# Performance work log

Measured on AMD Instinct MI355X. Metric: run time of the kernel, lower is better.

Reference implementation:

```python
import jax, jax.numpy as jnp
import numpy as np


def _blended_linear(h, W, b, blend):
    # Equivalent to building w[b] = sum_e blend[e,b]*W[e] (shape B,out,in)
    # and computing w[b] @ h[b] + sum_e blend[e,b]*b[e], without the huge
    # per-sample weight tensor.
    # h: (B, in), W: (E, out, in), b: (E, out), blend: (E, B) -> (B, out)
    y = jnp.einsum('eoi,bi->ebo', W, h)          # per-expert outputs
    y = jnp.einsum('eb,ebo->bo', blend, y)       # blend across experts
    return y + blend.T @ b                       # blended bias


def setup_inputs() -> dict:
    key = jax.random.key(0)
    ks = jax.random.split(key, 9)
    E, B = 8, 8192
    dims = [480, 512, 512, 363]
    inp = {
        'x': jax.random.normal(ks[0], (B, dims[0]), jnp.float32),
        'weight_blend': jax.random.uniform(ks[1], (E, B), jnp.float32),
        'W1': jax.random.normal(ks[2], (E, dims[1], dims[0]), jnp.float32) * 0.05,
        'b1': jax.random.normal(ks[3], (E, dims[1]), jnp.float32) * 0.05,
        'W2': jax.random.normal(ks[4], (E, dims[2], dims[1]), jnp.float32) * 0.05,
        'b2': jax.random.normal(ks[5], (E, dims[2]), jnp.float32) * 0.05,
        'W3': jax.random.normal(ks[6], (E, dims[3], dims[2]), jnp.float32) * 0.05,
        'b3': jax.random.normal(ks[7], (E, dims[3]), jnp.float32) * 0.05,
        'batch_size': B,
    }
    return inp


def reference(x, weight_blend, W1, b1, W2, b2, W3, b3, batch_size):
    # Dropout layers are identity in eval mode; final_ac=True -> softmax.
    h = _blended_linear(x, W1, b1, weight_blend)
    h = jax.nn.elu(h)
    h = _blended_linear(h, W2, b2, weight_blend)
    h = jax.nn.elu(h)
    h = _blended_linear(h, W3, b3, weight_blend)
    return jax.nn.softmax(h, axis=-1)
```

## Files before the change

kernel.cpp:

```cpp
#include <hip/hip_runtime.h>
#include <cstdint>

#define E_EXP 8
#define BATCH 8192
#define D0 480
#define D1 512
#define D2 512
#define D3 363
#define KP 512
#define N3PAD 384

typedef _Float16 f16x8 __attribute__((ext_vector_type(8)));
typedef float f32x4 __attribute__((ext_vector_type(4)));
typedef unsigned short u16;
typedef u16 u16x8 __attribute__((ext_vector_type(8)));

__device__ __forceinline__ u16 f2h(float f) {
    _Float16 h = (_Float16)f;
    return __builtin_bit_cast(u16, h);
}

__device__ __forceinline__ void async16(const u16* g, u16* s) {
    __builtin_amdgcn_global_load_lds(
        reinterpret_cast<const __attribute__((address_space(1))) void*>(
            reinterpret_cast<uintptr_t>(g)),
        reinterpret_cast<__attribute__((address_space(3))) void*>(
            reinterpret_cast<uintptr_t>(s)),
        16, 0, 0);
}

__device__ __forceinline__ void pack_seg(const float* __restrict__ src,
                                         u16* __restrict__ dst,
                                         int OUT_src, int OUTP, int IN_src) {
    int total = E_EXP * OUTP * 128;
    int in4 = IN_src >> 2;
    for (int idx = blockIdx.x * blockDim.x + threadIdx.x; idx < total;
         idx += gridDim.x * blockDim.x) {
        int e = idx / (OUTP * 128);
        int r = idx - e * OUTP * 128;
        int o = r >> 7;
        int k4 = r & 127;
        ushort4 w;
        if (o < OUT_src && k4 < in4) {
            const float4 v = *reinterpret_cast<const float4*>(
                src + ((size_t)e * OUT_src + o) * IN_src + (k4 << 2));
            w.x = f2h(v.x); w.y = f2h(v.y); w.z = f2h(v.z); w.w = f2h(v.w);
        } else {
            w.x = 0; w.y = 0; w.z = 0; w.w = 0;
        }
        *reinterpret_cast<ushort4*>(dst + ((size_t)e * OUTP + o) * KP + (k4 << 2)) = w;
    }
}

__global__ void pack_all(const float* __restrict__ W1, const float* __restrict__ W2,
                         const float* __restrict__ W3, u16* __restrict__ wf1,
                         u16* __restrict__ wf2, u16* __restrict__ wf3) {
    pack_seg(W1, wf1, 512, 512, D0);
    pack_seg(W2, wf2, 512, 512, D1);
    pack_seg(W3, wf3, D3, N3PAD, D2);
}

__global__ void pad_x(const float* __restrict__ x, u16* __restrict__ xp) {
    int total = BATCH * 128;
    for (int idx = blockIdx.x * blockDim.x + threadIdx.x; idx < total;
         idx += gridDim.x * blockDim.x) {
        int b = idx >> 7, k4 = idx & 127;
        ushort4 w;
        if (k4 < 120) {
            const float4 v = *reinterpret_cast<const float4*>(
                x + (size_t)b * D0 + (k4 << 2));
            w.x = f2h(v.x); w.y = f2h(v.y); w.z = f2h(v.z); w.w = f2h(v.w);
        } else {
            w.x = 0; w.y = 0; w.z = 0; w.w = 0;
        }
        *reinterpret_cast<ushort4*>(xp + (size_t)b * KP + (k4 << 2)) = w;
    }
}

__global__ __launch_bounds__(512, 2) void gemm_all(
    const u16* __restrict__ A, const u16* __restrict__ Bw,
    const float* __restrict__ blend, const float* __restrict__ bias,
    u16* __restrict__ out, int OUTP, int OUTR, int nbn, int mode) {
    __shared__ __align__(16) u16 S[49152];
    const int tid = threadIdx.x;
    const int w = tid >> 6, lane = tid & 63;
    const int wm2 = w & 3, wn2 = w >> 2;
    const int q = lane >> 4, l15 = lane & 15;

    const int id = blockIdx.x;
    const int xcd = id & 7;
    const int j = id >> 3;
    const int bm = ((j & 3) << 3) + xcd;
    const int bn = j >> 2;

    f32x4 acc[4][2];
#pragma unroll
    for (int mi = 0; mi < 4; ++mi)
#pragma unroll
        for (int ni = 0; ni < 2; ++ni) acc[mi][ni] = (f32x4){0.f, 0.f, 0.f, 0.f};

    _Float16 blh[8][4];
#pragma unroll
    for (int e = 0; e < 8; ++e)
#pragma unroll
        for (int mi = 0; mi < 4; ++mi)
            blh[e][mi] = (_Float16)blend[e * BATCH + bm * 256 + wm2 * 64 +
                                         mi * 16 + l15];

    const int l4r = lane >> 2;
    const int l4s = lane & 3;
    const int ks8 = (l4s ^ (l4r & 3)) << 3;
    const size_t EST = (size_t)OUTP * KP;
    const u16* gA0 = A + (size_t)(bm * 256 + w * 32 + l4r) * KP + ks8;
    const u16* gB0 = Bw + (size_t)w * EST + (size_t)(bn * 64 + l4r) * KP + ks8;
    const size_t R16 = (size_t)16 * KP;
    const int aBase = w * 1024;
    const int bBase = 8192 + w * 2048;

    const int ra = (q ^ (l15 & 3)) << 3;
    const int arow[4] = {(wm2 * 64 + 0 * 16 + l15) * 32 + ra,
                         (wm2 * 64 + 1 * 16 + l15) * 32 + ra,
                         (wm2 * 64 + 2 * 16 + l15) * 32 + ra,
                         (wm2 * 64 + 3 * 16 + l15) * 32 + ra};
    const int brow0 = (wn2 * 32 + l15) * 32 + ra;
    const int brow1 = (wn2 * 32 + 16 + l15) * 32 + ra;

    auto stage = [&](int kt, int p) {
        const int ko = kt << 5;
        u16* buf = S + p * 24576;
        async16(gA0 + ko, buf + aBase);
        async16(gA0 + R16 + ko, buf + aBase + 512);
        async16(gB0 + ko, buf + bBase);
        async16(gB0 + R16 + ko, buf + bBase + 512);
        async16(gB0 + 2 * R16 + ko, buf + bBase + 1024);
        async16(gB0 + 3 * R16 + ko, buf + bBase + 1536);
    };

    stage(0, 0);
    __syncthreads();

#pragma unroll 2
    for (int kt = 0; kt < 16; ++kt) {
        const int p = kt & 1;
        if (kt < 15) stage(kt + 1, p ^ 1);
        const u16* As_ = S + p * 24576;
        const u16* Bs_ = As_ + 8192;
        f16x8 af[4];
#pragma unroll
        for (int mi = 0; mi < 4; ++mi)
            af[mi] = *reinterpret_cast<const f16x8*>(&As_[arow[mi]]);
#pragma unroll
        for (int e = 0; e < 8; ++e) {
            f16x8 bf0 = *reinterpret_cast<const f16x8*>(&Bs_[e * 2048 + brow0]);
            f16x8 bf1 = *reinterpret_cast<const f16x8*>(&Bs_[e * 2048 + brow1]);
#pragma unroll
            for (int mi = 0; mi < 4; ++mi) {
                f16x8 as = af[mi] * blh[e][mi];
                acc[mi][0] = __builtin_amdgcn_mfma_f32_16x16x32_f16(
                    as, bf0, acc[mi][0], 0, 0, 0);
                acc[mi][1] = __builtin_amdgcn_mfma_f32_16x16x32_f16(
                    as, bf1, acc[mi][1], 0, 0, 0);
            }
        }
        __syncthreads();
    }

    float* Blf = reinterpret_cast<float*>(S);
    float* Bif = reinterpret_cast<float*>(S + 16384);
    for (int idx = tid; idx < 2048; idx += 512) {
        int e = idx >> 8, r = idx & 255;
        Blf[r * 8 + e] = blend[e * BATCH + bm * 256 + r];
    }
    {
        int e = tid >> 6, c = tid & 63;
        int cg = bn * 64 + c;
        Bif[c * 8 + e] = (cg < OUTR) ? bias[e * OUTR + cg] : 0.f;
    }
    __syncthreads();
#pragma unroll
    for (int mi = 0; mi < 4; ++mi) {
#pragma unroll
        for (int ni = 0; ni < 2; ++ni) {
            int col_l = wn2 * 32 + ni * 16 + l15;
            int gcol = bn * 64 + col_l;
#pragma unroll
            for (int r = 0; r < 4; ++r) {
                int rl = wm2 * 64 + mi * 16 + q * 4 + r;
                float bb = 0.f;
#pragma unroll
                for (int e = 0; e < 8; ++e)
                    bb += Blf[rl * 8 + e] * Bif[col_l * 8 + e];
                float v = acc[mi][ni][r] + bb;
                if (mode == 0) v = v > 0.f ? v : expm1f(v);
                out[(size_t)(bm * 256 + rl) * OUTP + gcol] = f2h(v);
            }
        }
    }
}

__global__ __launch_bounds__(128) void softmax_rows(
    const u16* __restrict__ P, float* __restrict__ out) {
    const int b = blockIdx.x;
    const int tid = threadIdx.x, lane = tid & 63, w = tid >> 6;
    float v[3];
    int n = 0;
    float mx = -3.4e38f;
    for (int i = tid; i < D3; i += 128) {
        float s = (float)*reinterpret_cast<const _Float16*>(
            P + (size_t)b * N3PAD + i);
        v[n] = s; mx = fmaxf(mx, s); ++n;
    }
#pragma unroll
    for (int off = 32; off >= 1; off >>= 1) mx = fmaxf(mx, __shfl_xor(mx, off, 64));
    __shared__ float sm[4];
    if (lane == 0) sm[w] = mx;
    __syncthreads();
    mx = fmaxf(sm[0], sm[1]);
    float s = 0.f;
    for (int jj = 0; jj < n; ++jj) { v[jj] = expf(v[jj] - mx); s += v[jj]; }
#pragma unroll
    for (int off = 32; off >= 1; off >>= 1) s += __shfl_xor(s, off, 64);
    if (lane == 0) sm[2 + w] = s;
    __syncthreads();
    float inv = 1.f / (sm[2] + sm[3]);
    n = 0;
    for (int i = tid; i < D3; i += 128) { out[(size_t)b * D3 + i] = v[n] * inv; ++n; }
}

extern "C" void kernel_launch(void* const* d_in, const int* in_sizes, int n_in,
                              void* d_out, int out_size, void* d_ws, size_t ws_size,
                              hipStream_t stream) {
    const float* x = (const float*)d_in[0];
    const float* blend = (const float*)d_in[1];
    const float* W1 = (const float*)d_in[2];
    const float* b1 = (const float*)d_in[3];
    const float* W2 = (const float*)d_in[4];
    const float* b2 = (const float*)d_in[5];
    const float* W3 = (const float*)d_in[6];
    const float* b3 = (const float*)d_in[7];
    float* outp = (float*)d_out;

    char* ws = (char*)d_ws;
    u16* wf1 = (u16*)ws; ws += (size_t)E_EXP * 512 * KP * 2;
    u16* wf2 = (u16*)ws; ws += (size_t)E_EXP * 512 * KP * 2;
    u16* wf3 = (u16*)ws; ws += (size_t)E_EXP * N3PAD * KP * 2;
    u16* xp = (u16*)ws;  ws += (size_t)BATCH * KP * 2;
    u16* h1 = (u16*)ws;  ws += (size_t)BATCH * KP * 2;
    u16* h2 = (u16*)ws;  ws += (size_t)BATCH * KP * 2;
    u16* P = (u16*)ws;

    pack_all<<<1024, 256, 0, stream>>>(W1, W2, W3, wf1, wf2, wf3);
    pad_x<<<2048, 256, 0, stream>>>(x, xp);

    gemm_all<<<32 * 8, 512, 0, stream>>>(xp, wf1, blend, b1, h1, 512, 512, 8, 0);
    gemm_all<<<32 * 8, 512, 0, stream>>>(h1, wf2, blend, b2, h2, 512, 512, 8, 0);
    gemm_all<<<32 * 6, 512, 0, stream>>>(h2, wf3, blend, b3, P, N3PAD, D3, 6, 1);
    softmax_rows<<<BATCH, 128, 0, stream>>>(P, outp);
}
```

Baseline: 215.2 us.

## Switch blended GEMM to 32x32x16 MFMA with matching LDS swizzle

Replaces the 16x16x32 MFMA tiling with 32x32x16 MFMAs. The two k-halves go into separate accumulators that are summed in the epilogue, and the LDS read offsets and XOR swizzle are changed to fit the new fragment layout. The epilogue pads the blend and bias scratch arrays to stride 9 to avoid bank conflicts, and it hoists the per-column bias values into registers. The larger MFMA shape is meant to raise matrix-core throughput and reduce LDS fragment reads per FLOP. It doubles the accumulator work in the epilogue and risks layout mismatches.

```diff
diff --git a/kernel.cpp b/kernel.cpp
--- a/kernel.cpp
+++ b/kernel.cpp
@@ -11,9 +11,8 @@
 #define N3PAD 384
 
 typedef _Float16 f16x8 __attribute__((ext_vector_type(8)));
-typedef float f32x4 __attribute__((ext_vector_type(4)));
+typedef float f32x16 __attribute__((ext_vector_type(16)));
 typedef unsigned short u16;
-typedef u16 u16x8 __attribute__((ext_vector_type(8)));
 
 __device__ __forceinline__ u16 f2h(float f) {
     _Float16 h = (_Float16)f;
@@ -85,7 +84,7 @@
     const int tid = threadIdx.x;
     const int w = tid >> 6, lane = tid & 63;
     const int wm2 = w & 3, wn2 = w >> 2;
-    const int q = lane >> 4, l15 = lane & 15;
+    const int l31 = lane & 31, q2 = lane >> 5;
 
     const int id = blockIdx.x;
     const int xcd = id & 7;
@@ -93,23 +92,25 @@
     const int bm = ((j & 3) << 3) + xcd;
     const int bn = j >> 2;
 
-    f32x4 acc[4][2];
-#pragma unroll
-    for (int mi = 0; mi < 4; ++mi)
-#pragma unroll
-        for (int ni = 0; ni < 2; ++ni) acc[mi][ni] = (f32x4){0.f, 0.f, 0.f, 0.f};
-
-    _Float16 blh[8][4];
+    f32x16 acc[2][2];
+#pragma unroll
+    for (int mg = 0; mg < 2; ++mg)
+#pragma unroll
+        for (int kk = 0; kk < 2; ++kk)
+#pragma unroll
+            for (int i = 0; i < 16; ++i) acc[mg][kk][i] = 0.f;
+
+    _Float16 blh[8][2];
 #pragma unroll
     for (int e = 0; e < 8; ++e)
 #pragma unroll
-        for (int mi = 0; mi < 4; ++mi)
-            blh[e][mi] = (_Float16)blend[e * BATCH + bm * 256 + wm2 * 64 +
-                                         mi * 16 + l15];
+        for (int mg = 0; mg < 2; ++mg)
+            blh[e][mg] = (_Float16)blend[e * BATCH + bm * 256 + wm2 * 64 +
+                                         mg * 32 + l31];
 
     const int l4r = lane >> 2;
     const int l4s = lane & 3;
-    const int ks8 = (l4s ^ (l4r & 3)) << 3;
+    const int ks8 = (l4s ^ ((l4r >> 1) & 3)) << 3;
     const size_t EST = (size_t)OUTP * KP;
     const u16* gA0 = A + (size_t)(bm * 256 + w * 32 + l4r) * KP + ks8;
     const u16* gB0 = Bw + (size_t)w * EST + (size_t)(bn * 64 + l4r) * KP + ks8;
@@ -117,13 +118,24 @@
     const int aBase = w * 1024;
     const int bBase = 8192 + w * 2048;
 
-    const int ra = (q ^ (l15 & 3)) << 3;
-    const int arow[4] = {(wm2 * 64 + 0 * 16 + l15) * 32 + ra,
-                         (wm2 * 64 + 1 * 16 + l15) * 32 + ra,
-                         (wm2 * 64 + 2 * 16 + l15) * 32 + ra,
-                         (wm2 * 64 + 3 * 16 + l15) * 32 + ra};
-    const int brow0 = (wn2 * 32 + l15) * 32 + ra;
-    const int brow1 = (wn2 * 32 + 16 + l15) * 32 + ra;
+    int aoff[2][2], boff[2];
+#pragma unroll
+    for (int mg = 0; mg < 2; ++mg) {
+        int r = wm2 * 64 + mg * 32 + l31;
+        int base = (r >> 4) * 512 + (r & 15) * 32;
+        int swz = (r >> 1) & 3;
+#pragma unroll
+        for (int kk = 0; kk < 2; ++kk)
+            aoff[mg][kk] = base + (((kk * 2 + q2) ^ swz) << 3);
+    }
+    {
+        int r = wn2 * 32 + l31;
+        int base = (r >> 4) * 512 + (r & 15) * 32;
+        int swz = (r >> 1) & 3;
+#pragma unroll
+        for (int kk = 0; kk < 2; ++kk)
+            boff[kk] = base + (((kk * 2 + q2) ^ swz) << 3);
+    }
 
     auto stage = [&](int kt, int p) {
         const int ko = kt << 5;
@@ -145,55 +157,59 @@
         if (kt < 15) stage(kt + 1, p ^ 1);
         const u16* As_ = S + p * 24576;
         const u16* Bs_ = As_ + 8192;
-        f16x8 af[4];
-#pragma unroll
-        for (int mi = 0; mi < 4; ++mi)
-            af[mi] = *reinterpret_cast<const f16x8*>(&As_[arow[mi]]);
+        f16x8 af[2][2];
+#pragma unroll
+        for (int mg = 0; mg < 2; ++mg)
+#pragma unroll
+            for (int kk = 0; kk < 2; ++kk)
+                af[mg][kk] = *reinterpret_cast<const f16x8*>(&As_[aoff[mg][kk]]);
 #pragma unroll
         for (int e = 0; e < 8; ++e) {
-            f16x8 bf0 = *reinterpret_cast<const f16x8*>(&Bs_[e * 2048 + brow0]);
-            f16x8 bf1 = *reinterpret_cast<const f16x8*>(&Bs_[e * 2048 + brow1]);
-#pragma unroll
-            for (int mi = 0; mi < 4; ++mi) {
-                f16x8 as = af[mi] * blh[e][mi];
-                acc[mi][0] = __builtin_amdgcn_mfma_f32_16x16x32_f16(
-                    as, bf0, acc[mi][0], 0, 0, 0);
-                acc[mi][1] = __builtin_amdgcn_mfma_f32_16x16x32_f16(
-                    as, bf1, acc[mi][1], 0, 0, 0);
+            f16x8 bf0 = *reinterpret_cast<const f16x8*>(&Bs_[e * 2048 + boff[0]]);
+            f16x8 bf1 = *reinterpret_cast<const f16x8*>(&Bs_[e * 2048 + boff[1]]);
+#pragma unroll
+            for (int mg = 0; mg < 2; ++mg) {
+                f16x8 a0 = af[mg][0] * blh[e][mg];
+                acc[mg][0] = __builtin_amdgcn_mfma_f32_32x32x16_f16(
+                    a0, bf0, acc[mg][0], 0, 0, 0);
+                f16x8 a1 = af[mg][1] * blh[e][mg];
+                acc[mg][1] = __builtin_amdgcn_mfma_f32_32x32x16_f16(
+                    a1, bf1, acc[mg][1], 0, 0, 0);
             }
         }
         __syncthreads();
     }
 
     float* Blf = reinterpret_cast<float*>(S);
-    float* Bif = reinterpret_cast<float*>(S + 16384);
+    float* Bif = reinterpret_cast<float*>(S + 8192);
     for (int idx = tid; idx < 2048; idx += 512) {
         int e = idx >> 8, r = idx & 255;
-        Blf[r * 8 + e] = blend[e * BATCH + bm * 256 + r];
+        Blf[r * 9 + e] = blend[e * BATCH + bm * 256 + r];
     }
     {
         int e = tid >> 6, c = tid & 63;
         int cg = bn * 64 + c;
-        Bif[c * 8 + e] = (cg < OUTR) ? bias[e * OUTR + cg] : 0.f;
-    }
-    __syncthreads();
-#pragma unroll
-    for (int mi = 0; mi < 4; ++mi) {
-#pragma unroll
-        for (int ni = 0; ni < 2; ++ni) {
-            int col_l = wn2 * 32 + ni * 16 + l15;
-            int gcol = bn * 64 + col_l;
-#pragma unroll
-            for (int r = 0; r < 4; ++r) {
-                int rl = wm2 * 64 + mi * 16 + q * 4 + r;
-                float bb = 0.f;
-#pragma unroll
-                for (int e = 0; e < 8; ++e)
-                    bb += Blf[rl * 8 + e] * Bif[col_l * 8 + e];
-                float v = acc[mi][ni][r] + bb;
-                if (mode == 0) v = v > 0.f ? v : expm1f(v);
-                out[(size_t)(bm * 256 + rl) * OUTP + gcol] = f2h(v);
-            }
+        Bif[c * 9 + e] = (cg < OUTR) ? bias[e * OUTR + cg] : 0.f;
+    }
+    __syncthreads();
+
+    const int col_l = wn2 * 32 + l31;
+    const int gcol = bn * 64 + col_l;
+    float bif[8];
+#pragma unroll
+    for (int e = 0; e < 8; ++e) bif[e] = Bif[col_l * 9 + e];
+#pragma unroll
+    for (int mg = 0; mg < 2; ++mg) {
+#pragma unroll
+        for (int reg = 0; reg < 16; ++reg) {
+            int rloc = (reg & 3) + ((reg >> 2) << 3) + (q2 << 2);
+            int rl = wm2 * 64 + mg * 32 + rloc;
+            float bb = 0.f;
+#pragma unroll
+            for (int e = 0; e < 8; ++e) bb += Blf[rl * 9 + e] * bif[e];
+            float v = acc[mg][0][reg] + acc[mg][1][reg] + bb;
+            if (mode == 0) v = v > 0.f ? v : expm1f(v);
+            out[(size_t)(bm * 256 + rl) * OUTP + gcol] = f2h(v);
         }
     }
 }
```

Result: no change. 217.4 us (+1.0%).
